# Optimization experiments

Measured on AMD Instinct MI355X. Metric: run time of the kernel, lower is better.

## Reference

```python
import jax, jax.numpy as jnp
import numpy as np
import math

B, L, D, H = 4, 2048, 1024, 16
DK = D // H


def setup_inputs() -> dict:
    key = jax.random.key(0)
    ks = jax.random.split(key, 12)
    scale = math.sqrt(6.0 / (D + D))  # xavier_uniform for square Linear
    def lin(k):
        return jax.random.uniform(k, (D, D), jnp.float32, -scale, scale)
    inp = {
        "query": jax.random.normal(ks[0], (B, L, D), jnp.float32),
        "key": jax.random.normal(ks[1], (B, L, D), jnp.float32),
        "value": jax.random.normal(ks[2], (B, L, D), jnp.float32),
        "Wq": lin(ks[3]), "bq": jnp.zeros((D,), jnp.float32),
        "Wk": lin(ks[4]), "bk": jnp.zeros((D,), jnp.float32),
        "Wv": lin(ks[5]), "bv": jnp.zeros((D,), jnp.float32),
        "Wo": lin(ks[6]), "bo": jnp.zeros((D,), jnp.float32),
        # causal mask: True means masked (hide future positions)
        "attn_mask": jnp.triu(jnp.ones((L, L), dtype=bool), k=1),
    }
    return inp


def reference(query, key, value, Wq, bq, Wk, bk, Wv, bv, Wo, bo, attn_mask):
    def proj(x, W, b):
        # torch Linear: x @ W.T + b ; then split heads -> [B, H, L, DK]
        y = jnp.einsum('bld,ed->ble', x, W) + b
        return y.reshape(B, L, H, DK).transpose(0, 2, 1, 3)

    q = proj(query, Wq, bq)
    k = proj(key, Wk, bk)
    v = proj(value, Wv, bv)

    scores = jnp.einsum('bhqd,bhkd->bhqk', q, k) / jnp.sqrt(jnp.float32(DK))
    scores = jnp.where(attn_mask[None, None, :, :], jnp.float32(-jnp.inf), scores)
    p_attn = jax.nn.softmax(scores, axis=-1)  # dropout p=0 (eval)

    ctx = jnp.einsum('bhqk,bhkd->bhqd', p_attn, v)
    ctx = ctx.transpose(0, 2, 1, 3).reshape(B, L, D)
    out = jnp.einsum('bld,ed->ble', ctx, Wo) + bo
    return out
```

## Files before the change

kernel.cpp:

```cpp
#include <hip/hip_runtime.h>
#include <hip/hip_bf16.h>
#include <stdint.h>

typedef unsigned short u16;
typedef unsigned int u32;
typedef short short8 __attribute__((ext_vector_type(8)));
typedef float f32x4 __attribute__((ext_vector_type(4)));
typedef u32 u32x4 __attribute__((ext_vector_type(4)));
typedef u32 u32x2 __attribute__((ext_vector_type(2)));

#define DEV static __device__ __forceinline__

constexpr int Bsz = 4, Lseq = 2048, Dm = 1024, Hn = 16, Dk = 64;
constexpr float LOG2E = 1.44269504088896340736f;
constexpr float QSCALE = 0.125f * LOG2E;

DEV u16 f2bf(float x) {
    u32 u = __builtin_bit_cast(u32, x);
    return (u16)((u + 0x7fffu + ((u >> 16) & 1u)) >> 16);
}

DEV u32 pk2(float a, float b) {
    __hip_bfloat162 h = __float22bfloat162_rn(float2{a, b});
    u32 r;
    __builtin_memcpy(&r, &h, 4);
    return r;
}

DEV u32x4 ld8_cvt(const float* p) {
    f32x4 lo = *(const f32x4*)p;
    f32x4 hi = *(const f32x4*)(p + 4);
    u32x4 r;
    r[0] = pk2(lo[0], lo[1]);
    r[1] = pk2(lo[2], lo[3]);
    r[2] = pk2(hi[0], hi[1]);
    r[3] = pk2(hi[2], hi[3]);
    return r;
}

template <int MODE, int A32>
__global__ __launch_bounds__(256) void gemm_bt(
    const void* __restrict__ Xv, const float* __restrict__ W,
    const float* __restrict__ bias, void* __restrict__ Cout, int Kdim,
    float scale)
{
    __shared__ u16 At[2][128 * 32];
    __shared__ u16 Bt[2][128 * 32];

    const int tid = threadIdx.x;
    const int lane = tid & 63, wid = tid >> 6;
    const int wr = wid >> 1, wc = wid & 1;
    const int mbase = blockIdx.x * 128, nbase = blockIdx.y * 128;

    f32x4 acc[4][4];
#pragma unroll
    for (int i = 0; i < 4; i++)
#pragma unroll
        for (int j = 0; j < 4; j++) acc[i][j] = (f32x4)0.f;

    const int NT = Kdim >> 5;

    u32x4 va[2], vb[2];
#pragma unroll
    for (int i = 0; i < 2; i++) {
        int idx = i * 256 + tid;
        int row = idx >> 2, seg = idx & 3;
        if (A32)
            va[i] = ld8_cvt((const float*)Xv + (long)(mbase + row) * Kdim + seg * 8);
        else
            va[i] = *(const u32x4*)((const u16*)Xv + (long)(mbase + row) * Kdim + seg * 8);
        vb[i] = ld8_cvt(W + (long)(nbase + row) * Kdim + seg * 8);
    }
#pragma unroll
    for (int i = 0; i < 2; i++) {
        int idx = i * 256 + tid;
        *(u32x4*)&At[0][idx * 8] = va[i];
        *(u32x4*)&Bt[0][idx * 8] = vb[i];
    }
    __syncthreads();

    for (int kt = 0; kt < NT; kt++) {
        const int cur = kt & 1;
        const bool more = (kt + 1 < NT);
        if (more) {
#pragma unroll
            for (int i = 0; i < 2; i++) {
                int idx = i * 256 + tid;
                int row = idx >> 2, seg = idx & 3;
                long ko = (long)(kt + 1) * 32 + seg * 8;
                if (A32)
                    va[i] = ld8_cvt((const float*)Xv + (long)(mbase + row) * Kdim + ko);
                else
                    va[i] = *(const u32x4*)((const u16*)Xv + (long)(mbase + row) * Kdim + ko);
                vb[i] = ld8_cvt(W + (long)(nbase + row) * Kdim + ko);
            }
        }
        short8 af[4], bfr[4];
#pragma unroll
        for (int mf = 0; mf < 4; mf++)
            af[mf] = *(const short8*)&At[cur][(wr * 64 + mf * 16 + (lane & 15)) * 32 + (lane >> 4) * 8];
#pragma unroll
        for (int nf = 0; nf < 4; nf++)
            bfr[nf] = *(const short8*)&Bt[cur][(wc * 64 + nf * 16 + (lane & 15)) * 32 + (lane >> 4) * 8];
#pragma unroll
        for (int mf = 0; mf < 4; mf++)
#pragma unroll
            for (int nf = 0; nf < 4; nf++)
                acc[mf][nf] = __builtin_amdgcn_mfma_f32_16x16x32_bf16(af[mf], bfr[nf], acc[mf][nf], 0, 0, 0);
        if (more) {
#pragma unroll
            for (int i = 0; i < 2; i++) {
                int idx = i * 256 + tid;
                *(u32x4*)&At[cur ^ 1][idx * 8] = va[i];
                *(u32x4*)&Bt[cur ^ 1][idx * 8] = vb[i];
            }
        }
        __syncthreads();
    }

#pragma unroll
    for (int nf = 0; nf < 4; nf++) {
        const int n = nbase + wc * 64 + nf * 16 + (lane & 15);
        const float bv = bias[n];
#pragma unroll
        for (int mf = 0; mf < 4; mf++) {
            const int m0 = mbase + wr * 64 + mf * 16 + (lane >> 4) * 4;
#pragma unroll
            for (int r = 0; r < 4; r++) {
                const int m = m0 + r;
                const float v = (acc[mf][nf][r] + bv) * scale;
                if (MODE == 0) {
                    int b = m >> 11, l = m & 2047, h = n >> 6, dk = n & 63;
                    long addr = ((long)(b * Hn + h) * Lseq + l) * Dk + dk;
                    ((u16*)Cout)[addr] = f2bf(v);
                } else {
                    ((float*)Cout)[(long)m * Dm + n] = v;
                }
            }
        }
    }
}

__global__ __launch_bounds__(256) void attn_fwd(
    const u16* __restrict__ Qb, const u16* __restrict__ Kb,
    const u16* __restrict__ Vb, u16* __restrict__ Ctx)
{
    __shared__ u16 Kt[2][64 * 64];
    __shared__ u16 Vt[2][64 * 64];
    __shared__ u16 Pq[4][32 * 64];

    const int tid = threadIdx.x, lane = tid & 63, w = tid >> 6;
    const int qt = gridDim.y - 1 - blockIdx.y;
    const int bh = blockIdx.x;
    const long base = (long)bh * Lseq * Dk;
    const int qw = qt * 128 + w * 32;

    const int skv = tid >> 3, seg = tid & 7;

    short8 qfr[2][2];
#pragma unroll
    for (int qf = 0; qf < 2; qf++)
#pragma unroll
        for (int ks = 0; ks < 2; ks++) {
            int q = qw + qf * 16 + (lane & 15);
            int d0 = ks * 32 + (lane >> 4) * 8;
            qfr[qf][ks] = *(const short8*)(Qb + base + (long)q * Dk + d0);
        }

    f32x4 accT[4][2];
#pragma unroll
    for (int i = 0; i < 4; i++)
#pragma unroll
        for (int j = 0; j < 2; j++) accT[i][j] = (f32x4)0.f;
    float m_run[2] = {-__builtin_inff(), -__builtin_inff()};
    float l_run[2] = {0.f, 0.f};

    u32x4 kr[2], vr[2];
#pragma unroll
    for (int i = 0; i < 2; i++) {
        int kv = i * 32 + skv;
        kr[i] = *(const u32x4*)(Kb + base + (long)kv * Dk + seg * 8);
        vr[i] = *(const u32x4*)(Vb + base + (long)kv * Dk + seg * 8);
    }
#pragma unroll
    for (int i = 0; i < 2; i++) {
        int kv = i * 32 + skv;
        *(u32x4*)&Kt[0][kv * 64 + ((seg * 8) ^ ((kv & 7) << 3))] = kr[i];
        const u16* pv = (const u16*)&vr[i];
#pragma unroll
        for (int j = 0; j < 8; j++) {
            int d = seg * 8 + j;
            Vt[0][d * 64 + (kv ^ ((((d & 7) ^ (d >> 3)) & 7) << 3))] = pv[j];
        }
    }
    __syncthreads();

    const int nkv = qt * 2 + 2;
    const int myn = ((qw + 31) >> 6) + 1;

    for (int kvt = 0; kvt < nkv; kvt++) {
        const int cur = kvt & 1;
        const bool more = (kvt + 1 < nkv);
        const int kvbase = kvt * 64;

        if (more) {
#pragma unroll
            for (int i = 0; i < 2; i++) {
                int kv = i * 32 + skv;
                long row = (long)(kvbase + 64 + kv) * Dk;
                kr[i] = *(const u32x4*)(Kb + base + row + seg * 8);
                vr[i] = *(const u32x4*)(Vb + base + row + seg * 8);
            }
        }

        if (kvt < myn) {
            f32x4 st[4][2];
#pragma unroll
            for (int i = 0; i < 4; i++)
#pragma unroll
                for (int j = 0; j < 2; j++) st[i][j] = (f32x4)0.f;
#pragma unroll
            for (int ks = 0; ks < 2; ks++) {
                short8 kf[4];
#pragma unroll
                for (int kvf = 0; kvf < 4; kvf++) {
                    int row = kvf * 16 + (lane & 15);
                    int d0 = ks * 32 + (lane >> 4) * 8;
                    kf[kvf] = *(const short8*)&Kt[cur][row * 64 + (d0 ^ ((row & 7) << 3))];
                }
#pragma unroll
                for (int kvf = 0; kvf < 4; kvf++)
#pragma unroll
                    for (int qf = 0; qf < 2; qf++)
                        st[kvf][qf] = __builtin_amdgcn_mfma_f32_16x16x32_bf16(kf[kvf], qfr[qf][ks], st[kvf][qf], 0, 0, 0);
            }

            const bool need_mask = (kvbase + 63) > qw;
            if (need_mask) {
#pragma unroll
                for (int qf = 0; qf < 2; qf++) {
                    const int q = qw + qf * 16 + (lane & 15);
#pragma unroll
                    for (int kvf = 0; kvf < 4; kvf++)
#pragma unroll
                        for (int r = 0; r < 4; r++) {
                            int kv = kvbase + kvf * 16 + (lane >> 4) * 4 + r;
                            if (kv > q) st[kvf][qf][r] = -1e30f;
                        }
                }
            }

#pragma unroll
            for (int qf = 0; qf < 2; qf++) {
                float tmax = st[0][qf][0];
#pragma unroll
                for (int kvf = 0; kvf < 4; kvf++)
#pragma unroll
                    for (int r = 0; r < 4; r++) tmax = fmaxf(tmax, st[kvf][qf][r]);
                tmax = fmaxf(tmax, __shfl_xor(tmax, 16, 64));
                tmax = fmaxf(tmax, __shfl_xor(tmax, 32, 64));
                const float mnew = fmaxf(m_run[qf], tmax);
                const float sc = __builtin_exp2f(m_run[qf] - mnew);
                m_run[qf] = mnew;
                float tsum = 0.f;
#pragma unroll
                for (int kvf = 0; kvf < 4; kvf++)
#pragma unroll
                    for (int r = 0; r < 4; r++) {
                        float p = __builtin_exp2f(st[kvf][qf][r] - mnew);
                        st[kvf][qf][r] = p;
                        tsum += p;
                    }
                tsum += __shfl_xor(tsum, 16, 64);
                tsum += __shfl_xor(tsum, 32, 64);
                l_run[qf] = l_run[qf] * sc + tsum;
#pragma unroll
                for (int dkf = 0; dkf < 4; dkf++)
#pragma unroll
                    for (int r = 0; r < 4; r++) accT[dkf][qf][r] *= sc;
                const int qrow = qf * 16 + (lane & 15);
#pragma unroll
                for (int kvf = 0; kvf < 4; kvf++) {
                    u32x2 pk;
                    pk[0] = pk2(st[kvf][qf][0], st[kvf][qf][1]);
                    pk[1] = pk2(st[kvf][qf][2], st[kvf][qf][3]);
                    int kvi = (kvf * 16 + (lane >> 4) * 4) ^ ((lane & 7) << 3);
                    *(u32x2*)&Pq[w][qrow * 64 + kvi] = pk;
                }
            }

#pragma unroll
            for (int kf2 = 0; kf2 < 2; kf2++) {
                short8 vfr[4];
#pragma unroll
                for (int dkf = 0; dkf < 4; dkf++) {
                    int d = dkf * 16 + (lane & 15);
                    int kvi = (kf2 * 32 + (lane >> 4) * 8) ^ ((((d & 7) ^ (d >> 3)) & 7) << 3);
                    vfr[dkf] = *(const short8*)&Vt[cur][d * 64 + kvi];
                }
                short8 pfr[2];
#pragma unroll
                for (int qf = 0; qf < 2; qf++) {
                    int qrow = qf * 16 + (lane & 15);
                    int kvi = (kf2 * 32 + (lane >> 4) * 8) ^ ((lane & 7) << 3);
                    pfr[qf] = *(const short8*)&Pq[w][qrow * 64 + kvi];
                }
#pragma unroll
                for (int dkf = 0; dkf < 4; dkf++)
#pragma unroll
                    for (int qf = 0; qf < 2; qf++)
                        accT[dkf][qf] = __builtin_amdgcn_mfma_f32_16x16x32_bf16(vfr[dkf], pfr[qf], accT[dkf][qf], 0, 0, 0);
            }
        }

        if (more) {
#pragma unroll
            for (int i = 0; i < 2; i++) {
                int kv = i * 32 + skv;
                *(u32x4*)&Kt[cur ^ 1][kv * 64 + ((seg * 8) ^ ((kv & 7) << 3))] = kr[i];
                const u16* pv = (const u16*)&vr[i];
#pragma unroll
                for (int j = 0; j < 8; j++) {
                    int d = seg * 8 + j;
                    Vt[cur ^ 1][d * 64 + (kv ^ ((((d & 7) ^ (d >> 3)) & 7) << 3))] = pv[j];
                }
            }
        }
        __syncthreads();
    }

    const int b = bh >> 4, h = bh & 15;
#pragma unroll
    for (int qf = 0; qf < 2; qf++) {
        const float inv = 1.f / l_run[qf];
        const int q = qw + qf * 16 + (lane & 15);
#pragma unroll
        for (int dkf = 0; dkf < 4; dkf++) {
            const int dk0 = dkf * 16 + (lane >> 4) * 4;
            u32x2 o;
            o[0] = pk2(accT[dkf][qf][0] * inv, accT[dkf][qf][1] * inv);
            o[1] = pk2(accT[dkf][qf][2] * inv, accT[dkf][qf][3] * inv);
            long addr = ((long)b * Lseq + q) * Dm + h * Dk + dk0;
            *(u32x2*)(Ctx + addr) = o;
        }
    }
}

extern "C" void kernel_launch(void* const* d_in, const int* in_sizes, int n_in,
                              void* d_out, int out_size, void* d_ws, size_t ws_size,
                              hipStream_t stream)
{
    const float* query = (const float*)d_in[0];
    const float* key_  = (const float*)d_in[1];
    const float* value = (const float*)d_in[2];
    const float* Wq = (const float*)d_in[3];
    const float* bq = (const float*)d_in[4];
    const float* Wk = (const float*)d_in[5];
    const float* bk = (const float*)d_in[6];
    const float* Wv = (const float*)d_in[7];
    const float* bv = (const float*)d_in[8];
    const float* Wo = (const float*)d_in[9];
    const float* bo = (const float*)d_in[10];

    float* out = (float*)d_out;
    const size_t tens = (size_t)Bsz * Lseq * Dm;
    u16* Qb = (u16*)d_ws;
    u16* Kb = Qb + tens;
    u16* Vb = Kb + tens;
    u16* Cx = Vb + tens;

    dim3 g(64, 8), blk(256);
    gemm_bt<0, 1><<<g, blk, 0, stream>>>(query, Wq, bq, Qb, Dm, QSCALE);
    gemm_bt<0, 1><<<g, blk, 0, stream>>>(key_,  Wk, bk, Kb, Dm, 1.0f);
    gemm_bt<0, 1><<<g, blk, 0, stream>>>(value, Wv, bv, Vb, Dm, 1.0f);
    attn_fwd<<<dim3(Bsz * Hn, Lseq / 128), blk, 0, stream>>>(Qb, Kb, Vb, Cx);
    gemm_bt<1, 0><<<g, blk, 0, stream>>>(Cx, Wo, bo, out, Dm, 1.0f);
}
```

Baseline: 255.0 us.

## Pre-convert inputs to bf16, use direct global-to-LDS loads, lazy softmax rescale

Adds separate fp32-to-bf16 conversion kernels for the weights and activations, plus a new GEMM that stages bf16 tiles straight into LDS via global_load_lds. The attention kernel now loads K through global_load_lds too. Its softmax only rescales when the running max grows by more than 8, and the row-sum reduction moves to the end. Both kernels raise wave priority around the MFMA blocks. The aim is to cut in-GEMM conversion and register staging, at the cost of extra conversion launches and memory traffic. The new path is used only when the workspace is large enough.

```diff
diff --git a/kernel.cpp b/kernel.cpp
--- a/kernel.cpp
+++ b/kernel.cpp
@@ -38,6 +38,98 @@
     return r;
 }
 
+DEV void glds16(const void* g, void* l) {
+    __builtin_amdgcn_global_load_lds(
+        (const __attribute__((address_space(1))) void*)g,
+        (__attribute__((address_space(3))) void*)l, 16, 0, 0);
+}
+
+__global__ __launch_bounds__(256) void cvt_f2b(
+    const float* __restrict__ s, u16* __restrict__ d, int n8)
+{
+    int i = blockIdx.x * 256 + threadIdx.x;
+    if (i >= n8) return;
+    ((u32x4*)d)[i] = ld8_cvt(s + (long)i * 8);
+}
+
+template <int MODE>
+__global__ __launch_bounds__(256) void gemm_glds(
+    const u16* __restrict__ A, const u16* __restrict__ Bw,
+    const float* __restrict__ bias, void* __restrict__ Cout, float scale)
+{
+    __shared__ u16 At[2][128 * 32];
+    __shared__ u16 Bt[2][128 * 32];
+
+    const int tid = threadIdx.x;
+    const int lane = tid & 63, wid = tid >> 6;
+    const int wr = wid >> 1, wc = wid & 1;
+    const int mbase = blockIdx.x * 128, nbase = blockIdx.y * 128;
+
+    f32x4 acc[4][4];
+#pragma unroll
+    for (int i = 0; i < 4; i++)
+#pragma unroll
+        for (int j = 0; j < 4; j++) acc[i][j] = (f32x4)0.f;
+
+    const int srow = lane >> 2;
+    const int sseg = (lane & 3) * 8;
+
+    auto stage = [&](int kt, int buf) {
+#pragma unroll
+        for (int c = 0; c < 2; c++) {
+            const int sec = wid * 2 + c;
+            const long ko = (long)kt * 32 + sseg;
+            glds16(A + (long)(mbase + sec * 16 + srow) * Dm + ko, &At[buf][sec * 512]);
+            glds16(Bw + (long)(nbase + sec * 16 + srow) * Dm + ko, &Bt[buf][sec * 512]);
+        }
+    };
+
+    stage(0, 0);
+    __syncthreads();
+
+    for (int kt = 0; kt < 32; kt++) {
+        const int cur = kt & 1;
+        if (kt + 1 < 32) stage(kt + 1, cur ^ 1);
+        short8 af[4], bfr[4];
+#pragma unroll
+        for (int mf = 0; mf < 4; mf++)
+            af[mf] = *(const short8*)&At[cur][(wr * 64 + mf * 16 + (lane & 15)) * 32 + (lane >> 4) * 8];
+#pragma unroll
+        for (int nf = 0; nf < 4; nf++)
+            bfr[nf] = *(const short8*)&Bt[cur][(wc * 64 + nf * 16 + (lane & 15)) * 32 + (lane >> 4) * 8];
+        __builtin_amdgcn_s_setprio(1);
+#pragma unroll
+        for (int mf = 0; mf < 4; mf++)
+#pragma unroll
+            for (int nf = 0; nf < 4; nf++)
+                acc[mf][nf] = __builtin_amdgcn_mfma_f32_16x16x32_bf16(af[mf], bfr[nf], acc[mf][nf], 0, 0, 0);
+        __builtin_amdgcn_s_setprio(0);
+        __syncthreads();
+    }
+
+#pragma unroll
+    for (int nf = 0; nf < 4; nf++) {
+        const int n = nbase + wc * 64 + nf * 16 + (lane & 15);
+        const float bv = bias[n];
+#pragma unroll
+        for (int mf = 0; mf < 4; mf++) {
+            const int m0 = mbase + wr * 64 + mf * 16 + (lane >> 4) * 4;
+#pragma unroll
+            for (int r = 0; r < 4; r++) {
+                const int m = m0 + r;
+                const float v = (acc[mf][nf][r] + bv) * scale;
+                if (MODE == 0) {
+                    int b = m >> 11, l = m & 2047, h = n >> 6, dk = n & 63;
+                    long addr = ((long)(b * Hn + h) * Lseq + l) * Dk + dk;
+                    ((u16*)Cout)[addr] = f2bf(v);
+                } else {
+                    ((float*)Cout)[(long)m * Dm + n] = v;
+                }
+            }
+        }
+    }
+}
+
 template <int MODE, int A32>
 __global__ __launch_bounds__(256) void gemm_bt(
     const void* __restrict__ Xv, const float* __restrict__ W,
@@ -155,7 +247,9 @@
     const long base = (long)bh * Lseq * Dk;
     const int qw = qt * 128 + w * 32;
 
-    const int skv = tid >> 3, seg = tid & 7;
+    const int krow_in_w = lane >> 3;
+    const int kseg = lane & 7;
+    const int skv = tid >> 3, sdb = (tid & 7) * 8;
 
     short8 qfr[2][2];
 #pragma unroll
@@ -173,23 +267,30 @@
 #pragma unroll
         for (int j = 0; j < 2; j++) accT[i][j] = (f32x4)0.f;
     float m_run[2] = {-__builtin_inff(), -__builtin_inff()};
-    float l_run[2] = {0.f, 0.f};
-
-    u32x4 kr[2], vr[2];
+    float l_part[2] = {0.f, 0.f};
+
+    auto stage_k = [&](int kvbase, int buf) {
+#pragma unroll
+        for (int c = 0; c < 2; c++) {
+            int kv = w * 16 + c * 8 + krow_in_w;
+            int d0 = ((kseg ^ (kv & 7)) * 8);
+            glds16(Kb + base + (long)(kvbase + kv) * Dk + d0,
+                   &Kt[buf][(w * 16 + c * 8) * 64]);
+        }
+    };
+
+    u32x4 vr[2];
+    stage_k(0, 0);
+#pragma unroll
+    for (int i = 0; i < 2; i++)
+        vr[i] = *(const u32x4*)(Vb + base + (long)(i * 32 + skv) * Dk + sdb);
 #pragma unroll
     for (int i = 0; i < 2; i++) {
         int kv = i * 32 + skv;
-        kr[i] = *(const u32x4*)(Kb + base + (long)kv * Dk + seg * 8);
-        vr[i] = *(const u32x4*)(Vb + base + (long)kv * Dk + seg * 8);
-    }
-#pragma unroll
-    for (int i = 0; i < 2; i++) {
-        int kv = i * 32 + skv;
-        *(u32x4*)&Kt[0][kv * 64 + ((seg * 8) ^ ((kv & 7) << 3))] = kr[i];
         const u16* pv = (const u16*)&vr[i];
 #pragma unroll
         for (int j = 0; j < 8; j++) {
-            int d = seg * 8 + j;
+            int d = sdb + j;
             Vt[0][d * 64 + (kv ^ ((((d & 7) ^ (d >> 3)) & 7) << 3))] = pv[j];
         }
     }
@@ -204,13 +305,10 @@
         const int kvbase = kvt * 64;
 
         if (more) {
-#pragma unroll
-            for (int i = 0; i < 2; i++) {
-                int kv = i * 32 + skv;
-                long row = (long)(kvbase + 64 + kv) * Dk;
-                kr[i] = *(const u32x4*)(Kb + base + row + seg * 8);
-                vr[i] = *(const u32x4*)(Vb + base + row + seg * 8);
-            }
+            stage_k(kvbase + 64, cur ^ 1);
+#pragma unroll
+            for (int i = 0; i < 2; i++)
+                vr[i] = *(const u32x4*)(Vb + base + (long)(kvbase + 64 + i * 32 + skv) * Dk + sdb);
         }
 
         if (kvt < myn) {
@@ -219,6 +317,7 @@
             for (int i = 0; i < 4; i++)
 #pragma unroll
                 for (int j = 0; j < 2; j++) st[i][j] = (f32x4)0.f;
+            __builtin_amdgcn_s_setprio(1);
 #pragma unroll
             for (int ks = 0; ks < 2; ks++) {
                 short8 kf[4];
@@ -234,9 +333,9 @@
                     for (int qf = 0; qf < 2; qf++)
                         st[kvf][qf] = __builtin_amdgcn_mfma_f32_16x16x32_bf16(kf[kvf], qfr[qf][ks], st[kvf][qf], 0, 0, 0);
             }
-
-            const bool need_mask = (kvbase + 63) > qw;
-            if (need_mask) {
+            __builtin_amdgcn_s_setprio(0);
+
+            if ((kvbase + 63) > qw) {
 #pragma unroll
                 for (int qf = 0; qf < 2; qf++) {
                     const int q = qw + qf * 16 + (lane & 15);
@@ -259,25 +358,28 @@
                     for (int r = 0; r < 4; r++) tmax = fmaxf(tmax, st[kvf][qf][r]);
                 tmax = fmaxf(tmax, __shfl_xor(tmax, 16, 64));
                 tmax = fmaxf(tmax, __shfl_xor(tmax, 32, 64));
-                const float mnew = fmaxf(m_run[qf], tmax);
-                const float sc = __builtin_exp2f(m_run[qf] - mnew);
-                m_run[qf] = mnew;
-                float tsum = 0.f;
+                const bool norescale = __all((int)(tmax <= m_run[qf] + 8.f));
+                if (!norescale) {
+                    const float mnew = fmaxf(m_run[qf], tmax);
+                    const float sc = __builtin_exp2f(m_run[qf] - mnew);
+                    m_run[qf] = mnew;
+                    l_part[qf] *= sc;
+#pragma unroll
+                    for (int dkf = 0; dkf < 4; dkf++)
+#pragma unroll
+                        for (int r = 0; r < 4; r++) accT[dkf][qf][r] *= sc;
+                }
+                const float mq = m_run[qf];
+                float ts = 0.f;
 #pragma unroll
                 for (int kvf = 0; kvf < 4; kvf++)
 #pragma unroll
                     for (int r = 0; r < 4; r++) {
-                        float p = __builtin_exp2f(st[kvf][qf][r] - mnew);
+                        float p = __builtin_exp2f(st[kvf][qf][r] - mq);
                         st[kvf][qf][r] = p;
-                        tsum += p;
+                        ts += p;
                     }
-                tsum += __shfl_xor(tsum, 16, 64);
-                tsum += __shfl_xor(tsum, 32, 64);
-                l_run[qf] = l_run[qf] * sc + tsum;
-#pragma unroll
-                for (int dkf = 0; dkf < 4; dkf++)
-#pragma unroll
-                    for (int r = 0; r < 4; r++) accT[dkf][qf][r] *= sc;
+                l_part[qf] += ts;
                 const int qrow = qf * 16 + (lane & 15);
 #pragma unroll
                 for (int kvf = 0; kvf < 4; kvf++) {
@@ -305,11 +407,13 @@
                     int kvi = (kf2 * 32 + (lane >> 4) * 8) ^ ((lane & 7) << 3);
                     pfr[qf] = *(const short8*)&Pq[w][qrow * 64 + kvi];
                 }
+                __builtin_amdgcn_s_setprio(1);
 #pragma unroll
                 for (int dkf = 0; dkf < 4; dkf++)
 #pragma unroll
                     for (int qf = 0; qf < 2; qf++)
                         accT[dkf][qf] = __builtin_amdgcn_mfma_f32_16x16x32_bf16(vfr[dkf], pfr[qf], accT[dkf][qf], 0, 0, 0);
+                __builtin_amdgcn_s_setprio(0);
             }
         }
 
@@ -317,11 +421,10 @@
 #pragma unroll
             for (int i = 0; i < 2; i++) {
                 int kv = i * 32 + skv;
-                *(u32x4*)&Kt[cur ^ 1][kv * 64 + ((seg * 8) ^ ((kv & 7) << 3))] = kr[i];
                 const u16* pv = (const u16*)&vr[i];
 #pragma unroll
                 for (int j = 0; j < 8; j++) {
-                    int d = seg * 8 + j;
+                    int d = sdb + j;
                     Vt[cur ^ 1][d * 64 + (kv ^ ((((d & 7) ^ (d >> 3)) & 7) << 3))] = pv[j];
                 }
             }
@@ -332,7 +435,10 @@
     const int b = bh >> 4, h = bh & 15;
 #pragma unroll
     for (int qf = 0; qf < 2; qf++) {
-        const float inv = 1.f / l_run[qf];
+        float l = l_part[qf];
+        l += __shfl_xor(l, 16, 64);
+        l += __shfl_xor(l, 32, 64);
+        const float inv = 1.f / l;
         const int q = qw + qf * 16 + (lane & 15);
 #pragma unroll
         for (int dkf = 0; dkf < 4; dkf++) {
@@ -364,15 +470,43 @@
 
     float* out = (float*)d_out;
     const size_t tens = (size_t)Bsz * Lseq * Dm;
+    const size_t wTot = (size_t)Dm * Dm;
     u16* Qb = (u16*)d_ws;
     u16* Kb = Qb + tens;
     u16* Vb = Kb + tens;
-    u16* Cx = Vb + tens;
 
     dim3 g(64, 8), blk(256);
-    gemm_bt<0, 1><<<g, blk, 0, stream>>>(query, Wq, bq, Qb, Dm, QSCALE);
-    gemm_bt<0, 1><<<g, blk, 0, stream>>>(key_,  Wk, bk, Kb, Dm, 1.0f);
-    gemm_bt<0, 1><<<g, blk, 0, stream>>>(value, Wv, bv, Vb, Dm, 1.0f);
-    attn_fwd<<<dim3(Bsz * Hn, Lseq / 128), blk, 0, stream>>>(Qb, Kb, Vb, Cx);
-    gemm_bt<1, 0><<<g, blk, 0, stream>>>(Cx, Wo, bo, out, Dm, 1.0f);
-}
+    const size_t need = (4 * tens + 4 * wTot) * sizeof(u16);
+
+    if (ws_size >= need) {
+        u16* Xb = Vb + tens;
+        u16* Cx = Xb;
+        u16* Wqb = Xb + tens;
+        u16* Wkb = Wqb + wTot;
+        u16* Wvb = Wkb + wTot;
+        u16* Wob = Wvb + wTot;
+        const int n8w = (int)(wTot / 8), n8x = (int)(tens / 8);
+        const int gw = (n8w + 255) / 256, gx = (n8x + 255) / 256;
+        cvt_f2b<<<gw, blk, 0, stream>>>(Wq, Wqb, n8w);
+        cvt_f2b<<<gw, blk, 0, stream>>>(Wk, Wkb, n8w);
+        cvt_f2b<<<gw, blk, 0, stream>>>(Wv, Wvb, n8w);
+        cvt_f2b<<<gw, blk, 0, stream>>>(Wo, Wob, n8w);
+
+        cvt_f2b<<<gx, blk, 0, stream>>>(query, Xb, n8x);
+        gemm_glds<0><<<g, blk, 0, stream>>>(Xb, Wqb, bq, Qb, QSCALE);
+        cvt_f2b<<<gx, blk, 0, stream>>>(key_, Xb, n8x);
+        gemm_glds<0><<<g, blk, 0, stream>>>(Xb, Wkb, bk, Kb, 1.0f);
+        cvt_f2b<<<gx, blk, 0, stream>>>(value, Xb, n8x);
+        gemm_glds<0><<<g, blk, 0, stream>>>(Xb, Wvb, bv, Vb, 1.0f);
+
+        attn_fwd<<<dim3(Bsz * Hn, Lseq / 128), blk, 0, stream>>>(Qb, Kb, Vb, Cx);
+        gemm_glds<1><<<g, blk, 0, stream>>>(Cx, Wob, bo, out, 1.0f);
+    } else {
+        u16* Cx = Vb + tens;
+        gemm_bt<0, 1><<<g, blk, 0, stream>>>(query, Wq, bq, Qb, Dm, QSCALE);
+        gemm_bt<0, 1><<<g, blk, 0, stream>>>(key_,  Wk, bk, Kb, Dm, 1.0f);
+        gemm_bt<0, 1><<<g, blk, 0, stream>>>(value, Wv, bv, Vb, Dm, 1.0f);
+        attn_fwd<<<dim3(Bsz * Hn, Lseq / 128), blk, 0, stream>>>(Qb, Kb, Vb, Cx);
+        gemm_bt<1, 0><<<g, blk, 0, stream>>>(Cx, Wo, bo, out, Dm, 1.0f);
+    }
+}
```

Measured after the change: 251.8 us. No clear change (-1.3%).
